# Kernel optimization log

Hardware: AMD Instinct MI355X
Metric: run time of the kernel (lower is better)

The kernel has to match this reference:

```python
import jax, jax.numpy as jnp
import numpy as np

B, L, D, H, HD, K, MAXLEN = 4, 2048, 1024, 16, 64, 32, 2048


def setup_inputs() -> dict:
    key = jax.random.key(0)
    ks = jax.random.split(key, 8)
    s = 0.02  # init scale (stand-in for lecun-normal magnitude)
    return {
        "inputs_q": jax.random.normal(ks[0], (B, L, D), jnp.float32),
        "inputs_kv": jax.random.normal(ks[1], (B, L, D), jnp.float32),
        "Wv": jax.random.normal(ks[2], (D, H, HD), jnp.float32) * s,   # value DenseGeneral kernel
        "bv": jnp.zeros((H, HD), jnp.float32),                          # value bias
        "r1": jax.random.normal(ks[3], (H, MAXLEN, K), jnp.float32) * s,  # param 'random1'
        "r2": jax.random.normal(ks[4], (H, K, MAXLEN), jnp.float32) * s,  # param 'random2'
        "Wo": jax.random.normal(ks[5], (H, HD, D), jnp.float32) * s,   # output DenseGeneral kernel
        "bo": jnp.zeros((D,), jnp.float32),                             # output bias
    }


def reference(inputs_q, inputs_kv, Wv, bv, r1, r2, Wo, bo):
    # SynthesizerAttention with ignore_dot_product=True, mode='factorized_random',
    # no masks, deterministic (no dropout).
    qlen = inputs_q.shape[-2]
    kvlen = inputs_kv.shape[-2]
    # value projection: [B, Lkv, H, HD]; key=value, query=inputs_q (unused for scores)
    v = jnp.einsum('bnd,dhk->bnhk', inputs_kv, Wv) + bv
    # factorized random synthetic scores: [H, Lq, Lkv]
    syn = jnp.einsum('hlk,hkn->hln', r1[:, :qlen, :], r2[:, :, :kvlen])
    # softmax over the key/value axis (norm_dims in synthetic_attention).
    # Scores are batch-independent, so softmax once per head (broadcast over B).
    attn = jax.nn.softmax(syn, axis=-1)
    # weighted sum over values: [B, Lq, H, HD]
    y = jnp.einsum('hln,bnhk->blhk', attn, v)
    # output projection over (H, HD): [B, Lq, D]
    return jnp.einsum('blhk,hkd->bld', y, Wo) + bo
```

## Files before the change

### kernel.cpp

```cpp
#include <hip/hip_runtime.h>
#include <hip/hip_bf16.h>

#define LL 2048

typedef __bf16 bf16x8 __attribute__((ext_vector_type(8)));
typedef __bf16 bf16x4 __attribute__((ext_vector_type(4)));
typedef float f32x4 __attribute__((ext_vector_type(4)));

__device__ inline void gl_lds16(const __bf16* g, __bf16* l) {
    __builtin_amdgcn_global_load_lds((const __attribute__((address_space(1))) void*)g,
                                     (__attribute__((address_space(3))) void*)l, 16, 0, 0);
}

__global__ __launch_bounds__(256) void prep(const float* __restrict__ inputs_kv,
                                            const float* __restrict__ r1,
                                            const float* __restrict__ Wv,
                                            const float* __restrict__ Wo,
                                            const float* __restrict__ r2,
                                            __bf16* __restrict__ A1,
                                            __bf16* __restrict__ r1b,
                                            __bf16* __restrict__ Wvt,
                                            __bf16* __restrict__ Wot,
                                            __bf16* __restrict__ r2t) {
    __shared__ float Ls[32][65];
    int bid = blockIdx.x;
    const int tid = threadIdx.x;
    if (bid < 4608) {
        const float* in = (bid < 4096) ? inputs_kv : r1;
        __bf16* out = (bid < 4096) ? A1 : r1b;
        const int t = ((bid < 4096) ? bid : bid - 4096) * 256 + tid;
        const float4* in4 = (const float4*)in;
        float4 f0 = in4[t * 2], f1 = in4[t * 2 + 1];
        bf16x8 o;
        o[0] = (__bf16)f0.x; o[1] = (__bf16)f0.y; o[2] = (__bf16)f0.z; o[3] = (__bf16)f0.w;
        o[4] = (__bf16)f1.x; o[5] = (__bf16)f1.y; o[6] = (__bf16)f1.z; o[7] = (__bf16)f1.w;
        *(bf16x8*)&out[(size_t)t * 8] = o;
        return;
    }
    bid -= 4608;
    const float* in;
    __bf16* out;
    int R, C, r0, c0;
    if (bid < 512) {
        in = Wv; out = Wvt; R = 1024; C = 1024;
        c0 = (bid & 15) * 64; r0 = (bid >> 4) * 32;
    } else if (bid < 1024) {
        bid -= 512;
        in = Wo; out = Wot; R = 1024; C = 1024;
        c0 = (bid & 15) * 64; r0 = (bid >> 4) * 32;
    } else {
        bid -= 1024;
        const int bz = bid >> 5;
        in = r2 + (size_t)bz * 65536; out = r2t + (size_t)bz * 65536;
        R = 32; C = 2048;
        c0 = (bid & 31) * 64; r0 = 0;
    }
#pragma unroll
    for (int p = 0; p < 2; ++p) {
        int f = tid + 256 * p;
        int row = f >> 4, c4 = (f & 15) << 2;
        float4 v = *(const float4*)&in[(size_t)(r0 + row) * C + c0 + c4];
        Ls[row][c4 + 0] = v.x; Ls[row][c4 + 1] = v.y;
        Ls[row][c4 + 2] = v.z; Ls[row][c4 + 3] = v.w;
    }
    __syncthreads();
    const int orow = tid >> 2, rc = (tid & 3) << 3;
    bf16x8 o;
#pragma unroll
    for (int j = 0; j < 8; ++j) o[j] = (__bf16)Ls[rc + j][orow];
    *(bf16x8*)&out[(size_t)(c0 + orow) * R + r0 + rc] = o;
}

template <int MODE>
__global__ __launch_bounds__(256) void gemm_bt(const __bf16* __restrict__ A,
                                               const __bf16* __restrict__ Bt,
                                               const float* __restrict__ bias,
                                               void* __restrict__ Cout,
                                               int M, int N, int K) {
    __shared__ alignas(16) __bf16 As[128 * 32];
    __shared__ alignas(16) __bf16 Bs[128 * 32];
    const int tid = threadIdx.x;
    const int lane = tid & 63;
    const int wid = __builtin_amdgcn_readfirstlane(tid >> 6);
    const int row0 = blockIdx.y * 128, col0 = blockIdx.x * 128;
    const int l15 = lane & 15, quad = lane >> 4;
    const int wr = wid & 1, wc = wid >> 1;
    const int s0 = wid * 2, s1 = s0 + 1;

    const __bf16* ga0 = A + (size_t)(row0 + s0 * 16 + (lane >> 2)) * K + ((lane & 3) << 3);
    const __bf16* ga1 = ga0 + (size_t)16 * K;
    const __bf16* gb0 = Bt + (size_t)(col0 + s0 * 16 + (lane >> 2)) * K + ((lane & 3) << 3);
    const __bf16* gb1 = gb0 + (size_t)16 * K;
    __bf16* la0 = As + s0 * 512;
    __bf16* la1 = As + s1 * 512;
    __bf16* lb0 = Bs + s0 * 512;
    __bf16* lb1 = Bs + s1 * 512;

    f32x4 acc[4][4];
#pragma unroll
    for (int i = 0; i < 4; ++i)
#pragma unroll
        for (int j = 0; j < 4; ++j) acc[i][j] = (f32x4){0.f, 0.f, 0.f, 0.f};

    for (int k0 = 0; k0 < K; k0 += 32) {
        __syncthreads();
        gl_lds16(ga0 + k0, la0);
        gl_lds16(ga1 + k0, la1);
        gl_lds16(gb0 + k0, lb0);
        gl_lds16(gb1 + k0, lb1);
        __syncthreads();
        bf16x8 af[4], bfv[4];
#pragma unroll
        for (int i = 0; i < 4; ++i)
            af[i] = *(const bf16x8*)&As[(wr * 64 + i * 16 + l15) * 32 + quad * 8];
#pragma unroll
        for (int j = 0; j < 4; ++j)
            bfv[j] = *(const bf16x8*)&Bs[(wc * 64 + j * 16 + l15) * 32 + quad * 8];
#pragma unroll
        for (int i = 0; i < 4; ++i)
#pragma unroll
            for (int j = 0; j < 4; ++j)
                acc[i][j] = __builtin_amdgcn_mfma_f32_16x16x32_bf16(af[i], bfv[j], acc[i][j], 0, 0, 0);
    }

#pragma unroll
    for (int i = 0; i < 4; ++i) {
        const int rg = row0 + wr * 64 + i * 16 + quad * 4;
#pragma unroll
        for (int j = 0; j < 4; ++j) {
            const int cg = col0 + wc * 64 + j * 16 + l15;
            const float bb = bias[cg];
            if (MODE == 0) {
                const int b = rg >> 11, n = rg & 2047;
                const int h = cg >> 6, hd = cg & 63;
                const int nc = n >> 6, ks = (n >> 5) & 1, qj = (n >> 3) & 3, j0 = n & 7;
                const int jt = hd >> 4, fl = hd & 15;
                __bf16* V3 = (__bf16*)Cout;
                bf16x4 v;
#pragma unroll
                for (int r = 0; r < 4; ++r) v[r] = (__bf16)(acc[i][j][r] + bb);
                *(bf16x4*)&V3[(size_t)(((h * 32 + nc) * 4 + b) * 4096) +
                              (jt * 2 + ks) * 512 + fl * 32 + qj * 8 + j0] = v;
            } else {
                float* Cf = (float*)Cout;
#pragma unroll
                for (int r = 0; r < 4; ++r)
                    Cf[(size_t)(rg + r) * N + cg] = acc[i][j][r] + bb;
            }
        }
    }
}

__global__ __launch_bounds__(512) void attn_pv_v4(const __bf16* __restrict__ r1b,
                                                  const __bf16* __restrict__ r2t,
                                                  const __bf16* __restrict__ V3,
                                                  __bf16* __restrict__ yb) {
    __shared__ alignas(16) __bf16 Ps[2 * 2 * 4 * 1024];
    const int tid = threadIdx.x;
    const int lane = tid & 63;
    const int w = __builtin_amdgcn_readfirstlane(tid >> 6);
    const int b = w & 3, lh = w >> 2;
    const int l15 = lane & 15, quad = lane >> 4;
    const int id = blockIdx.x;
    const int h = id & 15;
    const int l0 = (id >> 4) << 7;

    bf16x8 bf1[4];
#pragma unroll
    for (int i = 0; i < 4; ++i)
        bf1[i] = *(const bf16x8*)&r1b[(size_t)(h * 2048 + l0 + lh * 64 + i * 16 + l15) * 32 + quad * 8];

    const __bf16* r2p = r2t + (size_t)(h * 2048 + b * 16 + l15) * 32 + quad * 8;
    const __bf16* vp = V3 + (size_t)((h * 32) * 4 + b) * 4096 + l15 * 32 + quad * 8;

    bf16x8 r2f = *(const bf16x8*)r2p;
    bf16x8 vpf[4][2];
#pragma unroll
    for (int jt = 0; jt < 4; ++jt)
#pragma unroll
        for (int ks = 0; ks < 2; ++ks)
            vpf[jt][ks] = *(const bf16x8*)(vp + (jt * 2 + ks) * 512);

    bf16x8 ones;
#pragma unroll
    for (int e = 0; e < 8; ++e) ones[e] = (__bf16)1.0f;

    f32x4 acc[4][4];
    f32x4 den[4];
#pragma unroll
    for (int i = 0; i < 4; ++i) {
        den[i] = (f32x4){0.f, 0.f, 0.f, 0.f};
#pragma unroll
        for (int j = 0; j < 4; ++j) acc[i][j] = (f32x4){0.f, 0.f, 0.f, 0.f};
    }
    const f32x4 zero4 = {0.f, 0.f, 0.f, 0.f};

    const int kw = b >> 1;
    const int jg = (b & 1) * 2 + (quad >> 1);
    const int q4 = (quad & 1) * 4;
    const int swz = (l15 >> 1) & 3;

    for (int c = 0; c < 32; ++c) {
        const int cn = (c < 31) ? 1 : 0;
        f32x4 s[4];
#pragma unroll
        for (int i = 0; i < 4; ++i)
            s[i] = __builtin_amdgcn_mfma_f32_16x16x32_bf16(r2f, bf1[i], zero4, 0, 0, 0);
        r2f = *(const bf16x8*)(r2p + (size_t)cn * 2048);
        __bf16* ps = &Ps[((c & 1) * 2 + lh) * 4096];
#pragma unroll
        for (int i = 0; i < 4; ++i) {
            bf16x4 p4;
#pragma unroll
            for (int r = 0; r < 4; ++r) p4[r] = (__bf16)__expf(s[i][r]);
            *(bf16x4*)&ps[i * 1024 + kw * 512 + l15 * 32 + ((jg ^ swz) << 3) + q4] = p4;
        }
        __syncthreads();
        bf16x8 pa[4][2];
#pragma unroll
        for (int i = 0; i < 4; ++i)
#pragma unroll
            for (int ks = 0; ks < 2; ++ks)
                pa[i][ks] = *(const bf16x8*)&ps[i * 1024 + ks * 512 + l15 * 32 + ((quad ^ swz) << 3)];
#pragma unroll
        for (int ks = 0; ks < 2; ++ks) {
#pragma unroll
            for (int i = 0; i < 4; ++i) {
#pragma unroll
                for (int jt = 0; jt < 4; ++jt)
                    acc[i][jt] = __builtin_amdgcn_mfma_f32_16x16x32_bf16(pa[i][ks], vpf[jt][ks],
                                                                         acc[i][jt], 0, 0, 0);
                den[i] = __builtin_amdgcn_mfma_f32_16x16x32_bf16(pa[i][ks], ones, den[i], 0, 0, 0);
            }
        }
        vp += cn * 16384;
#pragma unroll
        for (int jt = 0; jt < 4; ++jt)
#pragma unroll
            for (int ks = 0; ks < 2; ++ks)
                vpf[jt][ks] = *(const bf16x8*)(vp + (jt * 2 + ks) * 512);
    }

#pragma unroll
    for (int i = 0; i < 4; ++i) {
#pragma unroll
        for (int r = 0; r < 4; ++r) {
            const float iv = 1.0f / den[i][r];
            const int l = l0 + lh * 64 + i * 16 + quad * 4 + r;
            const size_t rowbase = ((size_t)b * LL + l) * 1024 + h * 64;
#pragma unroll
            for (int jt = 0; jt < 4; ++jt)
                yb[rowbase + jt * 16 + l15] = (__bf16)(acc[i][jt][r] * iv);
        }
    }
}

extern "C" void kernel_launch(void* const* d_in, const int* in_sizes, int n_in,
                              void* d_out, int out_size, void* d_ws, size_t ws_size,
                              hipStream_t stream) {
    const float* inputs_kv = (const float*)d_in[1];
    const float* Wv = (const float*)d_in[2];
    const float* bv = (const float*)d_in[3];
    const float* r1 = (const float*)d_in[4];
    const float* r2 = (const float*)d_in[5];
    const float* Wo = (const float*)d_in[6];
    const float* bo = (const float*)d_in[7];
    float* out = (float*)d_out;

    char* ws = (char*)d_ws;
    const size_t MB = 1024 * 1024;
    __bf16* A1  = (__bf16*)(ws);
    __bf16* Wvt = (__bf16*)(ws + 16 * MB);
    __bf16* Wot = (__bf16*)(ws + 18 * MB);
    __bf16* r1b = (__bf16*)(ws + 20 * MB);
    __bf16* r2t = (__bf16*)(ws + 22 * MB);
    __bf16* V3  = (__bf16*)(ws + 24 * MB);
    __bf16* yb  = (__bf16*)(ws + 40 * MB);

    prep<<<6144, 256, 0, stream>>>(inputs_kv, r1, Wv, Wo, r2, A1, r1b, Wvt, Wot, r2t);
    gemm_bt<0><<<dim3(8, 64), 256, 0, stream>>>(A1, Wvt, bv, V3, 8192, 1024, 1024);
    attn_pv_v4<<<256, 512, 0, stream>>>(r1b, r2t, V3, yb);
    gemm_bt<1><<<dim3(8, 64), 256, 0, stream>>>(yb, Wot, bo, out, 8192, 1024, 1024);
}
```

Measured before the change: 223.6 us.

## Software-pipeline score exp with PV MFMAs and remap GEMM block order

The attention kernel now computes the first chunk's scores before the loop. Inside the loop it loads P from LDS, computes the next chunk's scores, runs the PV MFMAs, and only then writes exp of the next scores into the other LDS buffer. This overlaps the exp/VALU work with MFMA execution and uses a raw s_barrier with an lgkmcnt wait in place of __syncthreads. Separately, the GEMM maps block IDs so consecutive blocks walk down rows within the same column tile, to improve L2 reuse of the B operand. The pipelining needs extra registers to hold the next scores and relies on correct double-buffer ordering.

Result: faster. 212.9 us (-4.8%).

```diff
diff --git a/kernel.cpp b/kernel.cpp
--- a/kernel.cpp
+++ b/kernel.cpp
@@ -82,7 +82,9 @@
     const int tid = threadIdx.x;
     const int lane = tid & 63;
     const int wid = __builtin_amdgcn_readfirstlane(tid >> 6);
-    const int row0 = blockIdx.y * 128, col0 = blockIdx.x * 128;
+    const int f = blockIdx.y * 8 + blockIdx.x;
+    const int g = (f & 7) * 64 + (f >> 3);
+    const int row0 = (g >> 3) * 128, col0 = (g & 7) * 128;
     const int l15 = lane & 15, quad = lane >> 4;
     const int wr = wid & 1, wc = wid >> 1;
     const int s0 = wid * 2, s1 = s0 + 1;
@@ -151,7 +153,7 @@
     }
 }
 
-__global__ __launch_bounds__(512) void attn_pv_v4(const __bf16* __restrict__ r1b,
+__global__ __launch_bounds__(512) void attn_pv_v7(const __bf16* __restrict__ r1b,
                                                   const __bf16* __restrict__ r2t,
                                                   const __bf16* __restrict__ V3,
                                                   __bf16* __restrict__ yb) {
@@ -200,28 +202,37 @@
     const int q4 = (quad & 1) * 4;
     const int swz = (l15 >> 1) & 3;
 
+    f32x4 s[4];
+#pragma unroll
+    for (int i = 0; i < 4; ++i)
+        s[i] = __builtin_amdgcn_mfma_f32_16x16x32_bf16(r2f, bf1[i], zero4, 0, 0, 0);
+    r2f = *(const bf16x8*)(r2p + 2048);
+    {
+        __bf16* ps = &Ps[lh * 4096];
+#pragma unroll
+        for (int i = 0; i < 4; ++i) {
+            bf16x4 p4;
+#pragma unroll
+            for (int r = 0; r < 4; ++r) p4[r] = (__bf16)__expf(s[i][r]);
+            *(bf16x4*)&ps[i * 1024 + kw * 512 + l15 * 32 + ((jg ^ swz) << 3) + q4] = p4;
+        }
+    }
+
     for (int c = 0; c < 32; ++c) {
-        const int cn = (c < 31) ? 1 : 0;
-        f32x4 s[4];
+        asm volatile("s_waitcnt lgkmcnt(0)" ::: "memory");
+        __builtin_amdgcn_s_barrier();
+        const __bf16* ps_r = &Ps[((c & 1) * 2 + lh) * 4096];
+        bf16x8 pa[4][2];
+#pragma unroll
+        for (int i = 0; i < 4; ++i)
+#pragma unroll
+            for (int ks = 0; ks < 2; ++ks)
+                pa[i][ks] = *(const bf16x8*)&ps_r[i * 1024 + ks * 512 + l15 * 32 + ((quad ^ swz) << 3)];
 #pragma unroll
         for (int i = 0; i < 4; ++i)
             s[i] = __builtin_amdgcn_mfma_f32_16x16x32_bf16(r2f, bf1[i], zero4, 0, 0, 0);
-        r2f = *(const bf16x8*)(r2p + (size_t)cn * 2048);
-        __bf16* ps = &Ps[((c & 1) * 2 + lh) * 4096];
-#pragma unroll
-        for (int i = 0; i < 4; ++i) {
-            bf16x4 p4;
-#pragma unroll
-            for (int r = 0; r < 4; ++r) p4[r] = (__bf16)__expf(s[i][r]);
-            *(bf16x4*)&ps[i * 1024 + kw * 512 + l15 * 32 + ((jg ^ swz) << 3) + q4] = p4;
-        }
-        __syncthreads();
-        bf16x8 pa[4][2];
-#pragma unroll
-        for (int i = 0; i < 4; ++i)
-#pragma unroll
-            for (int ks = 0; ks < 2; ++ks)
-                pa[i][ks] = *(const bf16x8*)&ps[i * 1024 + ks * 512 + l15 * 32 + ((quad ^ swz) << 3)];
+        const int i2 = (c < 30) ? (c + 2) : 31;
+        r2f = *(const bf16x8*)(r2p + (size_t)i2 * 2048);
 #pragma unroll
         for (int ks = 0; ks < 2; ++ks) {
 #pragma unroll
@@ -233,7 +244,16 @@
                 den[i] = __builtin_amdgcn_mfma_f32_16x16x32_bf16(pa[i][ks], ones, den[i], 0, 0, 0);
             }
         }
-        vp += cn * 16384;
+        __bf16* ps_w = &Ps[(((c + 1) & 1) * 2 + lh) * 4096];
+#pragma unroll
+        for (int i = 0; i < 4; ++i) {
+            bf16x4 p4;
+#pragma unroll
+            for (int r = 0; r < 4; ++r) p4[r] = (__bf16)__expf(s[i][r]);
+            *(bf16x4*)&ps_w[i * 1024 + kw * 512 + l15 * 32 + ((jg ^ swz) << 3) + q4] = p4;
+        }
+        const int cv = (c < 31) ? 1 : 0;
+        vp += cv * 16384;
 #pragma unroll
         for (int jt = 0; jt < 4; ++jt)
 #pragma unroll
@@ -279,6 +299,6 @@
 
     prep<<<6144, 256, 0, stream>>>(inputs_kv, r1, Wv, Wo, r2, A1, r1b, Wvt, Wot, r2t);
     gemm_bt<0><<<dim3(8, 64), 256, 0, stream>>>(A1, Wvt, bv, V3, 8192, 1024, 1024);
-    attn_pv_v4<<<256, 512, 0, stream>>>(r1b, r2t, V3, yb);
+    attn_pv_v7<<<256, 512, 0, stream>>>(r1b, r2t, V3, yb);
     gemm_bt<1><<<dim3(8, 64), 256, 0, stream>>>(yb, Wot, bo, out, 8192, 1024, 1024);
 }
```
